# Optimization experiments

Measured on AMD Instinct MI355X. Metric: run time of the kernel, lower is better.

Reference implementation:

```python
import jax, jax.numpy as jnp
import numpy as np

B, TQ, TP, D = 4, 512, 512, 256


def setup_inputs() -> dict:
    key = jax.random.key(0)
    ks = jax.random.split(key, 5)
    return {
        "q": jax.random.normal(ks[0], (B, TQ, D), dtype=jnp.float32),
        "p": jax.random.normal(ks[1], (B, TP, D), dtype=jnp.float32),
        "W0": jax.random.normal(ks[2], (D, D), dtype=jnp.float32) / np.sqrt(D),
        "W1": jax.random.normal(ks[3], (D, D), dtype=jnp.float32) / np.sqrt(D),
        "vc": jax.random.normal(ks[4], (D, 1), dtype=jnp.float32) * 0.05,
    }


def reference(q, p, W0, W1, vc):
    # q: [B,Tq,Dq], p: [B,Tp,Dp]
    prod_q = jnp.einsum('bqd,de->bqe', q, W0)   # [B,Tq,dim]
    prod_p = jnp.einsum('bpd,de->bpe', p, W1)   # [B,Tp,dim]
    # additive attention energies: tanh over broadcast sum [B,Tp,Tq,dim]
    energy = jnp.tanh(prod_p[:, :, None, :] + prod_q[:, None, :, :])
    scores = jnp.einsum('bpqe,e->bpq', energy, vc[:, 0])  # [B,Tp,Tq]
    # original softmax is over axis=-2 of [B,Tp,Tq], i.e. the Tp axis
    weights = jax.nn.softmax(scores, axis=1)   # [B,Tp,Tq]
    # weighted sum over the Tq axis of (tiled) q
    attention_q = jnp.einsum('bpq,bqd->bpd', weights, q)  # [B,Tp,Dq]
    return attention_q
```

## Files before the change

kernel.cpp:

```cpp
#include <hip/hip_runtime.h>

#define NB 4
#define TT 512
#define DD 256
#define K2L2E    2.885390081777927f
#define NEG2L2E (-2.885390081777927f)

#if defined(__has_builtin)
# if __has_builtin(__builtin_amdgcn_global_load_lds)
#  define HAS_GLL 1
# endif
#endif

typedef float v2f __attribute__((ext_vector_type(2)));

__device__ __forceinline__ v2f pk_fma(v2f a, v2f b, v2f c) {
#if defined(__has_builtin)
# if __has_builtin(__builtin_elementwise_fma)
    return __builtin_elementwise_fma(a, b, c);
# else
    v2f r; r.x = __builtin_fmaf(a.x, b.x, c.x); r.y = __builtin_fmaf(a.y, b.y, c.y); return r;
# endif
#else
    v2f r; r.x = __builtin_fmaf(a.x, b.x, c.x); r.y = __builtin_fmaf(a.y, b.y, c.y); return r;
#endif
}
__device__ __forceinline__ v2f splat2(float s) { v2f r; r.x = s; r.y = s; return r; }

__device__ __forceinline__ void stage16(const float* __restrict__ g, float* l) {
#ifdef HAS_GLL
    __builtin_amdgcn_global_load_lds((const __attribute__((address_space(1))) void*)g,
                                     (__attribute__((address_space(3))) void*)l, 16, 0, 0);
#else
    *(float4*)l = *(const float4*)g;
#endif
}

__global__ __launch_bounds__(256) void proj_exp_kernel(
    const float* __restrict__ qin, const float* __restrict__ pin,
    const float* __restrict__ W0, const float* __restrict__ W1,
    float* __restrict__ expQ, float* __restrict__ expP)
{
    const int blk = blockIdx.x;
    const int wh = blk >> 8, tid = blk & 255;
    const int m0 = (tid >> 2) * 32, n0 = (tid & 3) * 64;
    const float* A = wh ? pin : qin;
    const float* W = wh ? W1 : W0;

    __shared__ __align__(16) float As[32 * 34];
    __shared__ __align__(16) float Bs[32 * 64];

    const int t  = threadIdx.x;
    const int ar = t >> 3, ac4 = (t & 7) * 4;
    const int br = t >> 4, bc4 = (t & 15) * 4;
    const int tm = wh ? (t >> 4) : (t & 15);
    const int tn = wh ? (t & 15) : (t >> 4);

    const float* Ap = A + (long)(m0 + ar) * DD + ac4;

    float4 av  = *(const float4*)Ap;
    float4 bv0 = *(const float4*)(W + (long)br * DD + n0 + bc4);
    float4 bv1 = *(const float4*)(W + (long)(br + 16) * DD + n0 + bc4);

    v2f accv[2][2];
    accv[0][0] = splat2(0.f); accv[0][1] = splat2(0.f);
    accv[1][0] = splat2(0.f); accv[1][1] = splat2(0.f);

    for (int c = 0; c < 8; ++c) {
        As[(ac4 + 0) * 34 + ar] = av.x;
        As[(ac4 + 1) * 34 + ar] = av.y;
        As[(ac4 + 2) * 34 + ar] = av.z;
        As[(ac4 + 3) * 34 + ar] = av.w;
        *(float4*)&Bs[br * 64 + bc4]        = bv0;
        *(float4*)&Bs[(br + 16) * 64 + bc4] = bv1;
        __syncthreads();
        if (c < 7) {
            int k1 = (c + 1) * 32;
            av  = *(const float4*)(Ap + k1);
            bv0 = *(const float4*)(W + (long)(k1 + br) * DD + n0 + bc4);
            bv1 = *(const float4*)(W + (long)(k1 + 16 + br) * DD + n0 + bc4);
        }
        #pragma unroll
        for (int kk = 0; kk < 32; ++kk) {
            float2 a = *(const float2*)&As[kk * 34 + 2 * tm];
            float4 b = *(const float4*)&Bs[kk * 64 + 4 * tn];
            v2f b01; b01.x = b.x; b01.y = b.y;
            v2f b23; b23.x = b.z; b23.y = b.w;
            accv[0][0] = pk_fma(splat2(a.x), b01, accv[0][0]);
            accv[0][1] = pk_fma(splat2(a.x), b23, accv[0][1]);
            accv[1][0] = pk_fma(splat2(a.y), b01, accv[1][0]);
            accv[1][1] = pk_fma(splat2(a.y), b23, accv[1][1]);
        }
        __syncthreads();
    }

    float acc[2][4];
    #pragma unroll
    for (int i = 0; i < 2; ++i) {
        acc[i][0] = accv[i][0].x; acc[i][1] = accv[i][0].y;
        acc[i][2] = accv[i][1].x; acc[i][3] = accv[i][1].y;
    }

    const int bi = m0 >> 9;
    const int ml = m0 & 511;
    if (wh) {
        #pragma unroll
        for (int i = 0; i < 2; ++i) {
            float4 st;
            st.x = __builtin_amdgcn_exp2f(acc[i][0] * K2L2E);
            st.y = __builtin_amdgcn_exp2f(acc[i][1] * K2L2E);
            st.z = __builtin_amdgcn_exp2f(acc[i][2] * K2L2E);
            st.w = __builtin_amdgcn_exp2f(acc[i][3] * K2L2E);
            *(float4*)(expP + ((long)bi * TT + ml + 2 * tm + i) * DD + n0 + 4 * tn) = st;
        }
    } else {
        #pragma unroll
        for (int j = 0; j < 4; ++j) {
            int d = n0 + 4 * tn + j;
            float2 st;
            st.x = __builtin_amdgcn_exp2f(acc[0][j] * K2L2E);
            st.y = __builtin_amdgcn_exp2f(acc[1][j] * K2L2E);
            *(float2*)(expQ + ((long)bi * DD + d) * TT + ml + 2 * tm) = st;
        }
    }
}

__global__ __launch_bounds__(256) void score_kernel(
    const float* __restrict__ expP, const float* __restrict__ expQ,
    const float* __restrict__ vc, float* __restrict__ ebuf, float* __restrict__ lpart)
{
    const int b = blockIdx.z, pt = blockIdx.y, qt = blockIdx.x;
    const int p0 = pt * 64, q0 = qt * 64;
    const int t  = threadIdx.x;
    const int qx = t & 15;
    const int py = t >> 4;
    const int sw = py & 3;

    __shared__ __align__(16) float PA[2][64 * 64];
    __shared__ __align__(16) float QB[2][64 * 64];
    __shared__ __align__(16) float vcs[DD];

    const float* gP = expP + ((long)b * TT + p0) * DD;
    const float* gQ = expQ + (long)b * DD * TT + q0;

    #pragma unroll
    for (int s = 0; s < 4; ++s) {
        int f = t + 256 * s, pr = f >> 4, j = f & 15;
        stage16(gP + (long)pr * DD + 4 * (j ^ ((pr >> 2) & 3)), &PA[0][f * 4]);
    }
    #pragma unroll
    for (int s = 0; s < 4; ++s) {
        int f = t + 256 * s, d = f >> 4, o4 = (f & 15) * 4;
        stage16(gQ + (long)d * TT + o4, &QB[0][f * 4]);
    }
    vcs[t] = vc[t];
    __syncthreads();

    v2f acc[4][2];
    #pragma unroll
    for (int i = 0; i < 4; ++i) { acc[i][0] = splat2(0.f); acc[i][1] = splat2(0.f); }
    const v2f one = splat2(1.0f);

    int buf = 0;
    for (int c = 0; c < 4; ++c) {
        if (c < 3) {
            const float* gPc = gP + (c + 1) * 64;
            const float* gQc = gQ + (long)(c + 1) * 64 * TT;
            #pragma unroll
            for (int s = 0; s < 4; ++s) {
                int f = t + 256 * s, pr = f >> 4, j = f & 15;
                stage16(gPc + (long)pr * DD + 4 * (j ^ ((pr >> 2) & 3)), &PA[buf ^ 1][f * 4]);
            }
            #pragma unroll
            for (int s = 0; s < 4; ++s) {
                int f = t + 256 * s, d = f >> 4, o4 = (f & 15) * 4;
                stage16(gQc + (long)d * TT + o4, &QB[buf ^ 1][f * 4]);
            }
        }
        const float* vcb = &vcs[c * 64];
        const float* pa = &PA[buf][0];
        const float* qb = &QB[buf][0];
        #pragma unroll 4
        for (int dq = 0; dq < 16; ++dq) {
            float4 vq = *(const float4*)&vcb[4 * dq];
            float4 B0 = *(const float4*)&qb[(4 * dq + 0) * 64 + 4 * qx];
            float4 B1 = *(const float4*)&qb[(4 * dq + 1) * 64 + 4 * qx];
            float4 B2 = *(const float4*)&qb[(4 * dq + 2) * 64 + 4 * qx];
            float4 B3 = *(const float4*)&qb[(4 * dq + 3) * 64 + 4 * qx];
            const int sq = 4 * (dq ^ sw);
            float4 A0 = *(const float4*)&pa[(4 * py + 0) * 64 + sq];
            float4 A1 = *(const float4*)&pa[(4 * py + 1) * 64 + sq];
            float4 A2 = *(const float4*)&pa[(4 * py + 2) * 64 + sq];
            float4 A3 = *(const float4*)&pa[(4 * py + 3) * 64 + sq];
            v2f b0l; b0l.x = B0.x; b0l.y = B0.y;  v2f b0h; b0h.x = B0.z; b0h.y = B0.w;
            v2f b1l; b1l.x = B1.x; b1l.y = B1.y;  v2f b1h; b1h.x = B1.z; b1h.y = B1.w;
            v2f b2l; b2l.x = B2.x; b2l.y = B2.y;  v2f b2h; b2h.x = B2.z; b2h.y = B2.w;
            v2f b3l; b3l.x = B3.x; b3l.y = B3.y;  v2f b3h; b3h.x = B3.z; b3h.y = B3.w;
            #pragma unroll
            for (int i = 0; i < 4; ++i) {
                float4 a = (i == 0) ? A0 : (i == 1) ? A1 : (i == 2) ? A2 : A3;
                {
                    v2f f0 = pk_fma(splat2(a.x), b0l, one);
                    v2f f1 = pk_fma(splat2(a.y), b1l, one);
                    v2f f2 = pk_fma(splat2(a.z), b2l, one);
                    v2f f3 = pk_fma(splat2(a.w), b3l, one);
                    v2f t01 = f0 * f1;
                    v2f t23 = f2 * f3;
                    v2f den = t01 * t23;
                    v2f n01 = pk_fma(splat2(vq.x), f1, splat2(vq.y) * f0);
                    v2f n23 = pk_fma(splat2(vq.z), f3, splat2(vq.w) * f2);
                    v2f num = pk_fma(n01, t23, n23 * t01);
                    v2f r;
                    r.x = __builtin_amdgcn_rcpf(den.x);
                    r.y = __builtin_amdgcn_rcpf(den.y);
                    acc[i][0] = pk_fma(num, r, acc[i][0]);
                }
                {
                    v2f f0 = pk_fma(splat2(a.x), b0h, one);
                    v2f f1 = pk_fma(splat2(a.y), b1h, one);
                    v2f f2 = pk_fma(splat2(a.z), b2h, one);
                    v2f f3 = pk_fma(splat2(a.w), b3h, one);
                    v2f t01 = f0 * f1;
                    v2f t23 = f2 * f3;
                    v2f den = t01 * t23;
                    v2f n01 = pk_fma(splat2(vq.x), f1, splat2(vq.y) * f0);
                    v2f n23 = pk_fma(splat2(vq.z), f3, splat2(vq.w) * f2);
                    v2f num = pk_fma(n01, t23, n23 * t01);
                    v2f r;
                    r.x = __builtin_amdgcn_rcpf(den.x);
                    r.y = __builtin_amdgcn_rcpf(den.y);
                    acc[i][1] = pk_fma(num, r, acc[i][1]);
                }
            }
        }
        __syncthreads();
        buf ^= 1;
    }

    float* eb = ebuf + ((long)b * TT + p0) * TT + q0;
    float4 colp; colp.x = 0.f; colp.y = 0.f; colp.z = 0.f; colp.w = 0.f;
    #pragma unroll
    for (int i = 0; i < 4; ++i) {
        float4 ev;
        ev.x = __builtin_amdgcn_exp2f(acc[i][0].x * NEG2L2E);
        ev.y = __builtin_amdgcn_exp2f(acc[i][0].y * NEG2L2E);
        ev.z = __builtin_amdgcn_exp2f(acc[i][1].x * NEG2L2E);
        ev.w = __builtin_amdgcn_exp2f(acc[i][1].y * NEG2L2E);
        *(float4*)(eb + (long)(4 * py + i) * TT + 4 * qx) = ev;
        colp.x += ev.x; colp.y += ev.y; colp.z += ev.z; colp.w += ev.w;
    }
    float* scr = &PA[0][0];
    *(float4*)&scr[py * 64 + 4 * qx] = colp;
    __syncthreads();
    if (t < 64) {
        float s = 0.f;
        #pragma unroll
        for (int r = 0; r < 16; ++r) s += scr[r * 64 + t];
        lpart[((long)b * 8 + pt) * TT + q0 + t] = s;
    }
}

__global__ __launch_bounds__(256) void out_kernel(
    const float* __restrict__ ebuf, const float* __restrict__ qin,
    const float* __restrict__ lpart, float* __restrict__ out)
{
    const int b = blockIdx.z, pt = blockIdx.y, dt = blockIdx.x;
    const int m0 = pt * 32, n0 = dt * 32;
    const int t    = threadIdx.x;
    const int wv   = t >> 6;
    const int lane = t & 63;
    const int pg   = lane >> 3;
    const int dg   = lane & 7;

    __shared__ __align__(16) float smem[4 * 32 * 36];
    __shared__ float linv[TT];
    float* As = smem;
    float* Bs = smem + 64 * 36;

    #pragma unroll
    for (int s = 0; s < 2; ++s) {
        int qq = t + 256 * s;
        float sum = 0.f;
        #pragma unroll
        for (int pb = 0; pb < 8; ++pb) sum += lpart[((long)b * 8 + pb) * TT + qq];
        linv[qq] = __builtin_amdgcn_rcpf(sum);
    }
    __syncthreads();

    const float* Ab = ebuf + ((long)b * TT + m0) * TT;
    const float* Bb = qin + (long)b * TT * DD + n0;

    const int ar = t >> 3, ak4 = (t & 7) * 4;

    v2f acc[4][2];
    #pragma unroll
    for (int i = 0; i < 4; ++i) { acc[i][0] = splat2(0.f); acc[i][1] = splat2(0.f); }

    for (int c = 0; c < 8; ++c) {
        const int k0 = c * 64;
        #pragma unroll
        for (int s = 0; s < 2; ++s) {
            int f = t + 256 * s, kr = f >> 3, d4 = (f & 7) * 4;
            stage16(Bb + (long)(k0 + kr) * DD + d4, &Bs[f * 4]);
        }
        #pragma unroll
        for (int s = 0; s < 2; ++s) {
            int kq = ak4 + 32 * s;
            float4 a = *(const float4*)(Ab + (long)ar * TT + k0 + kq);
            float4 lv = *(const float4*)&linv[k0 + kq];
            As[(kq + 0) * 36 + ar] = a.x * lv.x;
            As[(kq + 1) * 36 + ar] = a.y * lv.y;
            As[(kq + 2) * 36 + ar] = a.z * lv.z;
            As[(kq + 3) * 36 + ar] = a.w * lv.w;
        }
        __syncthreads();
        const int kb = 16 * wv;
        #pragma unroll
        for (int u = 0; u < 16; ++u) {
            int kk = kb + u;
            float4 a  = *(const float4*)&As[kk * 36 + 4 * pg];
            float4 bq = *(const float4*)&Bs[kk * 32 + 4 * dg];
            v2f b0; b0.x = bq.x; b0.y = bq.y;
            v2f b1; b1.x = bq.z; b1.y = bq.w;
            acc[0][0] = pk_fma(splat2(a.x), b0, acc[0][0]);
            acc[0][1] = pk_fma(splat2(a.x), b1, acc[0][1]);
            acc[1][0] = pk_fma(splat2(a.y), b0, acc[1][0]);
            acc[1][1] = pk_fma(splat2(a.y), b1, acc[1][1]);
            acc[2][0] = pk_fma(splat2(a.z), b0, acc[2][0]);
            acc[2][1] = pk_fma(splat2(a.z), b1, acc[2][1]);
            acc[3][0] = pk_fma(splat2(a.w), b0, acc[3][0]);
            acc[3][1] = pk_fma(splat2(a.w), b1, acc[3][1]);
        }
        __syncthreads();
    }

    float* scr = smem;
    #pragma unroll
    for (int i = 0; i < 4; ++i) {
        *(v2f*)&scr[wv * 1152 + (4 * pg + i) * 36 + 4 * dg]     = acc[i][0];
        *(v2f*)&scr[wv * 1152 + (4 * pg + i) * 36 + 4 * dg + 2] = acc[i][1];
    }
    __syncthreads();
    {
        int pr = t >> 3, d0 = (t & 7) * 4;
        float4 s0 = *(const float4*)&scr[0 * 1152 + pr * 36 + d0];
        float4 s1 = *(const float4*)&scr[1 * 1152 + pr * 36 + d0];
        float4 s2 = *(const float4*)&scr[2 * 1152 + pr * 36 + d0];
        float4 s3 = *(const float4*)&scr[3 * 1152 + pr * 36 + d0];
        float4 v;
        v.x = (s0.x + s1.x) + (s2.x + s3.x);
        v.y = (s0.y + s1.y) + (s2.y + s3.y);
        v.z = (s0.z + s1.z) + (s2.z + s3.z);
        v.w = (s0.w + s1.w) + (s2.w + s3.w);
        *(float4*)(out + ((long)b * TT + m0 + pr) * DD + n0 + d0) = v;
    }
}

extern "C" void kernel_launch(void* const* d_in, const int* in_sizes, int n_in,
                              void* d_out, int out_size, void* d_ws, size_t ws_size,
                              hipStream_t stream) {
    const float* q  = (const float*)d_in[0];
    const float* p  = (const float*)d_in[1];
    const float* W0 = (const float*)d_in[2];
    const float* W1 = (const float*)d_in[3];
    const float* vc = (const float*)d_in[4];
    float* out = (float*)d_out;

    float* ws    = (float*)d_ws;
    float* expQ  = ws;
    float* expP  = ws + 524288;
    float* ebuf  = ws + 1048576;
    float* lpart = ws + 2097152;

    proj_exp_kernel<<<dim3(512), 256, 0, stream>>>(q, p, W0, W1, expQ, expP);
    score_kernel<<<dim3(8, 8, NB), 256, 0, stream>>>(expP, expQ, vc, ebuf, lpart);
    out_kernel<<<dim3(8, 16, NB), 256, 0, stream>>>(ebuf, q, lpart, out);
}
```

Before: 120.9 us.

## Double-buffer projection GEMM with 64-row tiles and async LDS staging of W

The projection kernel now computes 64x64 output tiles instead of 32x64, so each thread holds a 4x4 accumulator block and the grid halves to 256 blocks. Shared-memory tiles are double-buffered: the W tile is loaded directly into LDS with global_load_lds, and A is prefetched two chunks ahead, which removes one barrier per iteration. This raises per-thread data reuse but leaves fewer blocks to fill the GPU's compute units and uses more registers and LDS.

```diff
diff --git a/kernel.cpp b/kernel.cpp
--- a/kernel.cpp
+++ b/kernel.cpp
@@ -42,85 +42,107 @@
     float* __restrict__ expQ, float* __restrict__ expP)
 {
     const int blk = blockIdx.x;
-    const int wh = blk >> 8, tid = blk & 255;
-    const int m0 = (tid >> 2) * 32, n0 = (tid & 3) * 64;
+    const int wh = blk >> 7, tid = blk & 127;
+    const int m0 = (tid >> 2) * 64, n0 = (tid & 3) * 64;
     const float* A = wh ? pin : qin;
     const float* W = wh ? W1 : W0;
 
-    __shared__ __align__(16) float As[32 * 34];
-    __shared__ __align__(16) float Bs[32 * 64];
-
-    const int t  = threadIdx.x;
-    const int ar = t >> 3, ac4 = (t & 7) * 4;
+    __shared__ __align__(16) float As[2][32 * 68];
+    __shared__ __align__(16) float Bs[2][32 * 64];
+
+    const int t = threadIdx.x;
+    const int ar = t >> 2, ac4 = (t & 3) * 4;
     const int br = t >> 4, bc4 = (t & 15) * 4;
     const int tm = wh ? (t >> 4) : (t & 15);
     const int tn = wh ? (t & 15) : (t >> 4);
 
     const float* Ap = A + (long)(m0 + ar) * DD + ac4;
 
-    float4 av  = *(const float4*)Ap;
-    float4 bv0 = *(const float4*)(W + (long)br * DD + n0 + bc4);
-    float4 bv1 = *(const float4*)(W + (long)(br + 16) * DD + n0 + bc4);
-
-    v2f accv[2][2];
-    accv[0][0] = splat2(0.f); accv[0][1] = splat2(0.f);
-    accv[1][0] = splat2(0.f); accv[1][1] = splat2(0.f);
-
+    float4 av0 = *(const float4*)(Ap);
+    float4 av1 = *(const float4*)(Ap + 16);
+
+    stage16(W + (long)br * DD + n0 + bc4,        &Bs[0][t * 4]);
+    stage16(W + (long)(16 + br) * DD + n0 + bc4, &Bs[0][1024 + t * 4]);
+    #pragma unroll
+    for (int j = 0; j < 4; ++j) {
+        As[0][(ac4 + j) * 68 + ar]      = ((const float*)&av0)[j];
+        As[0][(16 + ac4 + j) * 68 + ar] = ((const float*)&av1)[j];
+    }
+    av0 = *(const float4*)(Ap + 32);
+    av1 = *(const float4*)(Ap + 48);
+    __syncthreads();
+
+    v2f acc[4][2];
+    #pragma unroll
+    for (int i = 0; i < 4; ++i) { acc[i][0] = splat2(0.f); acc[i][1] = splat2(0.f); }
+
+    int buf = 0;
     for (int c = 0; c < 8; ++c) {
-        As[(ac4 + 0) * 34 + ar] = av.x;
-        As[(ac4 + 1) * 34 + ar] = av.y;
-        As[(ac4 + 2) * 34 + ar] = av.z;
-        As[(ac4 + 3) * 34 + ar] = av.w;
-        *(float4*)&Bs[br * 64 + bc4]        = bv0;
-        *(float4*)&Bs[(br + 16) * 64 + bc4] = bv1;
-        __syncthreads();
         if (c < 7) {
-            int k1 = (c + 1) * 32;
-            av  = *(const float4*)(Ap + k1);
-            bv0 = *(const float4*)(W + (long)(k1 + br) * DD + n0 + bc4);
-            bv1 = *(const float4*)(W + (long)(k1 + 16 + br) * DD + n0 + bc4);
-        }
+            const int k1 = (c + 1) * 32;
+            stage16(W + (long)(k1 + br) * DD + n0 + bc4,      &Bs[buf ^ 1][t * 4]);
+            stage16(W + (long)(k1 + 16 + br) * DD + n0 + bc4, &Bs[buf ^ 1][1024 + t * 4]);
+            #pragma unroll
+            for (int j = 0; j < 4; ++j) {
+                As[buf ^ 1][(ac4 + j) * 68 + ar]      = ((const float*)&av0)[j];
+                As[buf ^ 1][(16 + ac4 + j) * 68 + ar] = ((const float*)&av1)[j];
+            }
+            if (c < 6) {
+                const int k2 = (c + 2) * 32;
+                av0 = *(const float4*)(Ap + k2);
+                av1 = *(const float4*)(Ap + k2 + 16);
+            }
+        }
+        const float* as = &As[buf][0];
+        const float* bs = &Bs[buf][0];
         #pragma unroll
         for (int kk = 0; kk < 32; ++kk) {
-            float2 a = *(const float2*)&As[kk * 34 + 2 * tm];
-            float4 b = *(const float4*)&Bs[kk * 64 + 4 * tn];
+            float4 a = *(const float4*)&as[kk * 68 + 4 * tm];
+            float4 b = *(const float4*)&bs[kk * 64 + 4 * tn];
             v2f b01; b01.x = b.x; b01.y = b.y;
             v2f b23; b23.x = b.z; b23.y = b.w;
-            accv[0][0] = pk_fma(splat2(a.x), b01, accv[0][0]);
-            accv[0][1] = pk_fma(splat2(a.x), b23, accv[0][1]);
-            accv[1][0] = pk_fma(splat2(a.y), b01, accv[1][0]);
-            accv[1][1] = pk_fma(splat2(a.y), b23, accv[1][1]);
+            acc[0][0] = pk_fma(splat2(a.x), b01, acc[0][0]);
+            acc[0][1] = pk_fma(splat2(a.x), b23, acc[0][1]);
+            acc[1][0] = pk_fma(splat2(a.y), b01, acc[1][0]);
+            acc[1][1] = pk_fma(splat2(a.y), b23, acc[1][1]);
+            acc[2][0] = pk_fma(splat2(a.z), b01, acc[2][0]);
+            acc[2][1] = pk_fma(splat2(a.z), b23, acc[2][1]);
+            acc[3][0] = pk_fma(splat2(a.w), b01, acc[3][0]);
+            acc[3][1] = pk_fma(splat2(a.w), b23, acc[3][1]);
         }
         __syncthreads();
-    }
-
-    float acc[2][4];
-    #pragma unroll
-    for (int i = 0; i < 2; ++i) {
-        acc[i][0] = accv[i][0].x; acc[i][1] = accv[i][0].y;
-        acc[i][2] = accv[i][1].x; acc[i][3] = accv[i][1].y;
+        buf ^= 1;
+    }
+
+    float ac[4][4];
+    #pragma unroll
+    for (int i = 0; i < 4; ++i) {
+        ac[i][0] = acc[i][0].x; ac[i][1] = acc[i][0].y;
+        ac[i][2] = acc[i][1].x; ac[i][3] = acc[i][1].y;
     }
 
     const int bi = m0 >> 9;
     const int ml = m0 & 511;
     if (wh) {
         #pragma unroll
-        for (int i = 0; i < 2; ++i) {
+        for (int i = 0; i < 4; ++i) {
             float4 st;
-            st.x = __builtin_amdgcn_exp2f(acc[i][0] * K2L2E);
-            st.y = __builtin_amdgcn_exp2f(acc[i][1] * K2L2E);
-            st.z = __builtin_amdgcn_exp2f(acc[i][2] * K2L2E);
-            st.w = __builtin_amdgcn_exp2f(acc[i][3] * K2L2E);
-            *(float4*)(expP + ((long)bi * TT + ml + 2 * tm + i) * DD + n0 + 4 * tn) = st;
+            st.x = __builtin_amdgcn_exp2f(ac[i][0] * K2L2E);
+            st.y = __builtin_amdgcn_exp2f(ac[i][1] * K2L2E);
+            st.z = __builtin_amdgcn_exp2f(ac[i][2] * K2L2E);
+            st.w = __builtin_amdgcn_exp2f(ac[i][3] * K2L2E);
+            *(float4*)(expP + (long)(m0 + 4 * tm + i) * DD + n0 + 4 * tn) = st;
         }
     } else {
         #pragma unroll
         for (int j = 0; j < 4; ++j) {
             int d = n0 + 4 * tn + j;
-            float2 st;
-            st.x = __builtin_amdgcn_exp2f(acc[0][j] * K2L2E);
-            st.y = __builtin_amdgcn_exp2f(acc[1][j] * K2L2E);
-            *(float2*)(expQ + ((long)bi * DD + d) * TT + ml + 2 * tm) = st;
+            float4 st;
+            st.x = __builtin_amdgcn_exp2f(ac[0][j] * K2L2E);
+            st.y = __builtin_amdgcn_exp2f(ac[1][j] * K2L2E);
+            st.z = __builtin_amdgcn_exp2f(ac[2][j] * K2L2E);
+            st.w = __builtin_amdgcn_exp2f(ac[3][j] * K2L2E);
+            *(float4*)(expQ + ((long)bi * DD + d) * TT + ml + 4 * tm) = st;
         }
     }
 }
@@ -372,7 +394,7 @@
     float* ebuf  = ws + 1048576;
     float* lpart = ws + 2097152;
 
-    proj_exp_kernel<<<dim3(512), 256, 0, stream>>>(q, p, W0, W1, expQ, expP);
+    proj_exp_kernel<<<dim3(256), 256, 0, stream>>>(q, p, W0, W1, expQ, expP);
     score_kernel<<<dim3(8, 8, NB), 256, 0, stream>>>(expP, expQ, vc, ebuf, lpart);
     out_kernel<<<dim3(8, 16, NB), 256, 0, stream>>>(ebuf, q, lpart, out);
 }
```

Measured after the change: 124.6 us. 3.1% more time.

## Split D reduction across two thread halves in score kernel

Applied to the files above, without the earlier changes.

Doubles the score kernel block to 512 threads, with each half accumulating tanh-weighted scores over half of the feature dimension. Full P and Q tiles are loaded into LDS up front instead of double-buffered chunks. The halves' partial sums are combined through shared memory before the exp and column-sum epilogue. This aims to increase waves per CU on a grid that only has one block per CU. In exchange it needs much larger LDS and gives up overlap of loads with compute.

```diff
diff --git a/kernel.cpp b/kernel.cpp
--- a/kernel.cpp
+++ b/kernel.cpp
@@ -125,137 +125,137 @@
     }
 }
 
-__global__ __launch_bounds__(256) void score_kernel(
+__global__ __launch_bounds__(512) void score_kernel(
     const float* __restrict__ expP, const float* __restrict__ expQ,
     const float* __restrict__ vc, float* __restrict__ ebuf, float* __restrict__ lpart)
 {
     const int b = blockIdx.z, pt = blockIdx.y, qt = blockIdx.x;
     const int p0 = pt * 64, q0 = qt * 64;
     const int t  = threadIdx.x;
-    const int qx = t & 15;
-    const int py = t >> 4;
-    const int sw = py & 3;
-
-    __shared__ __align__(16) float PA[2][64 * 64];
-    __shared__ __align__(16) float QB[2][64 * 64];
+    const int h  = t >> 8;
+    const int u  = t & 255;
+    const int qx = u & 15;
+    const int py = u >> 4;
+    const int sw = py & 7;
+
+    __shared__ __align__(16) float PA[64 * 256];
+    __shared__ __align__(16) float QB[256 * 64];
     __shared__ __align__(16) float vcs[DD];
 
     const float* gP = expP + ((long)b * TT + p0) * DD;
     const float* gQ = expQ + (long)b * DD * TT + q0;
 
     #pragma unroll
-    for (int s = 0; s < 4; ++s) {
-        int f = t + 256 * s, pr = f >> 4, j = f & 15;
-        stage16(gP + (long)pr * DD + 4 * (j ^ ((pr >> 2) & 3)), &PA[0][f * 4]);
-    }
-    #pragma unroll
-    for (int s = 0; s < 4; ++s) {
-        int f = t + 256 * s, d = f >> 4, o4 = (f & 15) * 4;
-        stage16(gQ + (long)d * TT + o4, &QB[0][f * 4]);
-    }
-    vcs[t] = vc[t];
+    for (int s = 0; s < 8; ++s) {
+        int f = t + 512 * s;
+        int pr = f >> 6, j = f & 63;
+        stage16(gP + (long)pr * DD + 4 * (j ^ ((pr >> 2) & 7)), &PA[f * 4]);
+    }
+    #pragma unroll
+    for (int s = 0; s < 8; ++s) {
+        int f = t + 512 * s;
+        int d = f >> 4, o4 = (f & 15) * 4;
+        stage16(gQ + (long)d * TT + o4, &QB[f * 4]);
+    }
+    if (t < DD) vcs[t] = vc[t];
     __syncthreads();
 
     v2f acc[4][2];
     #pragma unroll
     for (int i = 0; i < 4; ++i) { acc[i][0] = splat2(0.f); acc[i][1] = splat2(0.f); }
     const v2f one = splat2(1.0f);
-
-    int buf = 0;
-    for (int c = 0; c < 4; ++c) {
-        if (c < 3) {
-            const float* gPc = gP + (c + 1) * 64;
-            const float* gQc = gQ + (long)(c + 1) * 64 * TT;
-            #pragma unroll
-            for (int s = 0; s < 4; ++s) {
-                int f = t + 256 * s, pr = f >> 4, j = f & 15;
-                stage16(gPc + (long)pr * DD + 4 * (j ^ ((pr >> 2) & 3)), &PA[buf ^ 1][f * 4]);
+    const float* vcb = &vcs[h * 128];
+
+    #pragma unroll 4
+    for (int dq = 0; dq < 32; ++dq) {
+        const int dj = h * 32 + dq;
+        float4 vq = *(const float4*)&vcb[4 * dq];
+        const int sq = 4 * (dj ^ sw);
+        float4 A0 = *(const float4*)&PA[(4 * py + 0) * 256 + sq];
+        float4 A1 = *(const float4*)&PA[(4 * py + 1) * 256 + sq];
+        float4 A2 = *(const float4*)&PA[(4 * py + 2) * 256 + sq];
+        float4 A3 = *(const float4*)&PA[(4 * py + 3) * 256 + sq];
+        const int db = (4 * dj) * 64 + 4 * qx;
+        float4 B0 = *(const float4*)&QB[db];
+        float4 B1 = *(const float4*)&QB[db + 64];
+        float4 B2 = *(const float4*)&QB[db + 128];
+        float4 B3 = *(const float4*)&QB[db + 192];
+        v2f b0l; b0l.x = B0.x; b0l.y = B0.y;  v2f b0h; b0h.x = B0.z; b0h.y = B0.w;
+        v2f b1l; b1l.x = B1.x; b1l.y = B1.y;  v2f b1h; b1h.x = B1.z; b1h.y = B1.w;
+        v2f b2l; b2l.x = B2.x; b2l.y = B2.y;  v2f b2h; b2h.x = B2.z; b2h.y = B2.w;
+        v2f b3l; b3l.x = B3.x; b3l.y = B3.y;  v2f b3h; b3h.x = B3.z; b3h.y = B3.w;
+        #pragma unroll
+        for (int i = 0; i < 4; ++i) {
+            float4 a = (i == 0) ? A0 : (i == 1) ? A1 : (i == 2) ? A2 : A3;
+            {
+                v2f f0 = pk_fma(splat2(a.x), b0l, one);
+                v2f f1 = pk_fma(splat2(a.y), b1l, one);
+                v2f f2 = pk_fma(splat2(a.z), b2l, one);
+                v2f f3 = pk_fma(splat2(a.w), b3l, one);
+                v2f t01 = f0 * f1;
+                v2f t23 = f2 * f3;
+                v2f den = t01 * t23;
+                v2f n01 = pk_fma(splat2(vq.x), f1, splat2(vq.y) * f0);
+                v2f n23 = pk_fma(splat2(vq.z), f3, splat2(vq.w) * f2);
+                v2f num = pk_fma(n01, t23, n23 * t01);
+                v2f r;
+                r.x = __builtin_amdgcn_rcpf(den.x);
+                r.y = __builtin_amdgcn_rcpf(den.y);
+                acc[i][0] = pk_fma(num, r, acc[i][0]);
             }
-            #pragma unroll
-            for (int s = 0; s < 4; ++s) {
-                int f = t + 256 * s, d = f >> 4, o4 = (f & 15) * 4;
-                stage16(gQc + (long)d * TT + o4, &QB[buf ^ 1][f * 4]);
+            {
+                v2f f0 = pk_fma(splat2(a.x), b0h, one);
+                v2f f1 = pk_fma(splat2(a.y), b1h, one);
+                v2f f2 = pk_fma(splat2(a.z), b2h, one);
+                v2f f3 = pk_fma(splat2(a.w), b3h, one);
+                v2f t01 = f0 * f1;
+                v2f t23 = f2 * f3;
+                v2f den = t01 * t23;
+                v2f n01 = pk_fma(splat2(vq.x), f1, splat2(vq.y) * f0);
+                v2f n23 = pk_fma(splat2(vq.z), f3, splat2(vq.w) * f2);
+                v2f num = pk_fma(n01, t23, n23 * t01);
+                v2f r;
+                r.x = __builtin_amdgcn_rcpf(den.x);
+                r.y = __builtin_amdgcn_rcpf(den.y);
+                acc[i][1] = pk_fma(num, r, acc[i][1]);
             }
         }
-        const float* vcb = &vcs[c * 64];
-        const float* pa = &PA[buf][0];
-        const float* qb = &QB[buf][0];
-        #pragma unroll 4
-        for (int dq = 0; dq < 16; ++dq) {
-            float4 vq = *(const float4*)&vcb[4 * dq];
-            float4 B0 = *(const float4*)&qb[(4 * dq + 0) * 64 + 4 * qx];
-            float4 B1 = *(const float4*)&qb[(4 * dq + 1) * 64 + 4 * qx];
-            float4 B2 = *(const float4*)&qb[(4 * dq + 2) * 64 + 4 * qx];
-            float4 B3 = *(const float4*)&qb[(4 * dq + 3) * 64 + 4 * qx];
-            const int sq = 4 * (dq ^ sw);
-            float4 A0 = *(const float4*)&pa[(4 * py + 0) * 64 + sq];
-            float4 A1 = *(const float4*)&pa[(4 * py + 1) * 64 + sq];
-            float4 A2 = *(const float4*)&pa[(4 * py + 2) * 64 + sq];
-            float4 A3 = *(const float4*)&pa[(4 * py + 3) * 64 + sq];
-            v2f b0l; b0l.x = B0.x; b0l.y = B0.y;  v2f b0h; b0h.x = B0.z; b0h.y = B0.w;
-            v2f b1l; b1l.x = B1.x; b1l.y = B1.y;  v2f b1h; b1h.x = B1.z; b1h.y = B1.w;
-            v2f b2l; b2l.x = B2.x; b2l.y = B2.y;  v2f b2h; b2h.x = B2.z; b2h.y = B2.w;
-            v2f b3l; b3l.x = B3.x; b3l.y = B3.y;  v2f b3h; b3h.x = B3.z; b3h.y = B3.w;
-            #pragma unroll
-            for (int i = 0; i < 4; ++i) {
-                float4 a = (i == 0) ? A0 : (i == 1) ? A1 : (i == 2) ? A2 : A3;
-                {
-                    v2f f0 = pk_fma(splat2(a.x), b0l, one);
-                    v2f f1 = pk_fma(splat2(a.y), b1l, one);
-                    v2f f2 = pk_fma(splat2(a.z), b2l, one);
-                    v2f f3 = pk_fma(splat2(a.w), b3l, one);
-                    v2f t01 = f0 * f1;
-                    v2f t23 = f2 * f3;
-                    v2f den = t01 * t23;
-                    v2f n01 = pk_fma(splat2(vq.x), f1, splat2(vq.y) * f0);
-                    v2f n23 = pk_fma(splat2(vq.z), f3, splat2(vq.w) * f2);
-                    v2f num = pk_fma(n01, t23, n23 * t01);
-                    v2f r;
-                    r.x = __builtin_amdgcn_rcpf(den.x);
-                    r.y = __builtin_amdgcn_rcpf(den.y);
-                    acc[i][0] = pk_fma(num, r, acc[i][0]);
-                }
-                {
-                    v2f f0 = pk_fma(splat2(a.x), b0h, one);
-                    v2f f1 = pk_fma(splat2(a.y), b1h, one);
-                    v2f f2 = pk_fma(splat2(a.z), b2h, one);
-                    v2f f3 = pk_fma(splat2(a.w), b3h, one);
-                    v2f t01 = f0 * f1;
-                    v2f t23 = f2 * f3;
-                    v2f den = t01 * t23;
-                    v2f n01 = pk_fma(splat2(vq.x), f1, splat2(vq.y) * f0);
-                    v2f n23 = pk_fma(splat2(vq.z), f3, splat2(vq.w) * f2);
-                    v2f num = pk_fma(n01, t23, n23 * t01);
-                    v2f r;
-                    r.x = __builtin_amdgcn_rcpf(den.x);
-                    r.y = __builtin_amdgcn_rcpf(den.y);
-                    acc[i][1] = pk_fma(num, r, acc[i][1]);
-                }
-            }
-        }
-        __syncthreads();
-        buf ^= 1;
-    }
-
-    float* eb = ebuf + ((long)b * TT + p0) * TT + q0;
-    float4 colp; colp.x = 0.f; colp.y = 0.f; colp.z = 0.f; colp.w = 0.f;
-    #pragma unroll
-    for (int i = 0; i < 4; ++i) {
-        float4 ev;
-        ev.x = __builtin_amdgcn_exp2f(acc[i][0].x * NEG2L2E);
-        ev.y = __builtin_amdgcn_exp2f(acc[i][0].y * NEG2L2E);
-        ev.z = __builtin_amdgcn_exp2f(acc[i][1].x * NEG2L2E);
-        ev.w = __builtin_amdgcn_exp2f(acc[i][1].y * NEG2L2E);
-        *(float4*)(eb + (long)(4 * py + i) * TT + 4 * qx) = ev;
-        colp.x += ev.x; colp.y += ev.y; colp.z += ev.z; colp.w += ev.w;
-    }
-    float* scr = &PA[0][0];
-    *(float4*)&scr[py * 64 + 4 * qx] = colp;
+    }
+
+    __syncthreads();
+    float* scr = &PA[0];
+    if (h == 1) {
+        #pragma unroll
+        for (int i = 0; i < 4; ++i) {
+            float4 st;
+            st.x = acc[i][0].x; st.y = acc[i][0].y;
+            st.z = acc[i][1].x; st.w = acc[i][1].y;
+            *(float4*)&scr[(4 * py + i) * 64 + 4 * qx] = st;
+        }
+    }
+    __syncthreads();
+    float* scr2 = &QB[0];
+    if (h == 0) {
+        float* eb = ebuf + ((long)b * TT + p0) * TT + q0;
+        float4 colp; colp.x = 0.f; colp.y = 0.f; colp.z = 0.f; colp.w = 0.f;
+        #pragma unroll
+        for (int i = 0; i < 4; ++i) {
+            float4 o = *(const float4*)&scr[(4 * py + i) * 64 + 4 * qx];
+            float4 ev;
+            ev.x = __builtin_amdgcn_exp2f((acc[i][0].x + o.x) * NEG2L2E);
+            ev.y = __builtin_amdgcn_exp2f((acc[i][0].y + o.y) * NEG2L2E);
+            ev.z = __builtin_amdgcn_exp2f((acc[i][1].x + o.z) * NEG2L2E);
+            ev.w = __builtin_amdgcn_exp2f((acc[i][1].y + o.w) * NEG2L2E);
+            *(float4*)(eb + (long)(4 * py + i) * TT + 4 * qx) = ev;
+            colp.x += ev.x; colp.y += ev.y; colp.z += ev.z; colp.w += ev.w;
+        }
+        *(float4*)&scr2[py * 64 + 4 * qx] = colp;
+    }
     __syncthreads();
     if (t < 64) {
         float s = 0.f;
         #pragma unroll
-        for (int r = 0; r < 16; ++r) s += scr[r * 64 + t];
+        for (int r = 0; r < 16; ++r) s += scr2[r * 64 + t];
         lpart[((long)b * 8 + pt) * TT + q0 + t] = s;
     }
 }
@@ -373,6 +373,6 @@
     float* lpart = ws + 2097152;
 
     proj_exp_kernel<<<dim3(512), 256, 0, stream>>>(q, p, W0, W1, expQ, expP);
-    score_kernel<<<dim3(8, 8, NB), 256, 0, stream>>>(expP, expQ, vc, ebuf, lpart);
+    score_kernel<<<dim3(8, 8, NB), 512, 0, stream>>>(expP, expQ, vc, ebuf, lpart);
     out_kernel<<<dim3(8, 16, NB), 256, 0, stream>>>(ebuf, q, lpart, out);
 }
```

Result: faster. 117.2 us (-3.0%).
